# Performance work log

Hardware: AMD Instinct MI355X
Metric: run time of the kernel (lower is better)

The kernel has to match this reference:

```python
import jax, jax.numpy as jnp
import numpy as np

IN_FEATURES = 256
WIDTH = 512
GRID_POINTS = 32   # num control points
DEGREE = 3         # spline_order
BATCH = 8192
LN_EPS = 1e-5


def make_knots(num_ctrl_pts, degree):
    knot_count = num_ctrl_pts + degree + 1
    knots = np.zeros(knot_count, dtype=np.float32)
    knots[-(degree + 1):] = 1.0
    interior = knot_count - 2 * (degree + 1)
    if interior > 0:
        knots[degree + 1:degree + 1 + interior] = np.linspace(0.0, 1.0, interior + 2, dtype=np.float32)[1:-1]
    return jnp.asarray(knots)

KNOTS = make_knots(GRID_POINTS, DEGREE)  # [num_ctrl + degree + 1]


def bspline_basis(x, knots, degree):
    # x: [b, f] in [0,1]; returns [b, f, num_ctrl_pts]
    xe = x[..., None]                      # [b, f, 1]
    left = knots[:-1]
    right = knots[1:]
    basis = ((xe >= left) & (xe < right)).astype(x.dtype)            # [b,f,K-1]
    last = ((xe >= left[-1]) & (xe <= right[-1])).astype(x.dtype)    # [b,f,1]
    basis = jnp.concatenate([basis[..., :-1], last], axis=-1)
    for r in range(1, degree + 1):  # fixed small loop over spline order
        m = basis.shape[-1] - 1
        if m <= 0:
            break
        idx = np.arange(m)
        lk = knots[idx]                 # [m]
        rk = knots[idx + r + 1]
        d1 = knots[idx + r] - knots[idx]
        d2 = knots[idx + r + 1] - knots[idx + 1]
        s1 = jnp.where(d1 > 0, d1, 1.0)  # safe denominators (avoid nan in both where branches)
        s2 = jnp.where(d2 > 0, d2, 1.0)
        t1 = jnp.where(d1 > 0, (xe - lk) / s1, 0.0) * basis[..., :m]
        t2 = jnp.where(d2 > 0, (rk - xe) / s2, 0.0) * basis[..., 1:m + 1]
        basis = t1 + t2
    return basis


def setup_inputs() -> dict:
    key = jax.random.key(0)
    ks = jax.random.split(key, 8)
    coeff_init = np.sqrt(2.0 / (GRID_POINTS * IN_FEATURES)).astype(np.float32)
    return {
        "inputs": jax.random.normal(ks[0], (BATCH, IN_FEATURES), dtype=jnp.float32),
        "input_shift": jnp.zeros((IN_FEATURES,), dtype=jnp.float32),
        "input_log_scale": jnp.zeros((IN_FEATURES,), dtype=jnp.float32),
        "spline_coeffs": coeff_init * jax.random.normal(ks[1], (IN_FEATURES, GRID_POINTS, WIDTH), dtype=jnp.float32),
        "bias": jnp.zeros((WIDTH,), dtype=jnp.float32),
        "skip_w": jax.random.normal(ks[2], (IN_FEATURES, WIDTH), dtype=jnp.float32) / np.sqrt(IN_FEATURES).astype(np.float32),
        "skip_b": jnp.zeros((WIDTH,), dtype=jnp.float32),
        "ln_gamma": jnp.ones((WIDTH,), dtype=jnp.float32),
        "ln_beta": jnp.zeros((WIDTH,), dtype=jnp.float32),
    }


def reference(inputs, input_shift, input_log_scale, spline_coeffs, bias,
              skip_w, skip_b, ln_gamma, ln_beta):
    scale = jax.nn.softplus(input_log_scale) + 0.001
    normalised = jax.nn.sigmoid((inputs - input_shift) * scale)            # [b,f] in (0,1)
    basis = bspline_basis(normalised, KNOTS, DEGREE)                       # [b,f,g]
    spline_mix = jnp.einsum('bfg,fgw->bw', basis, spline_coeffs)
    linear_skip = inputs @ skip_w + skip_b
    combined = spline_mix + linear_skip + bias
    mu = jnp.mean(combined, axis=-1, keepdims=True)
    var = jnp.mean(jnp.square(combined - mu), axis=-1, keepdims=True)
    normed = (combined - mu) * jax.lax.rsqrt(var + LN_EPS) * ln_gamma + ln_beta
    return jax.nn.gelu(normed, approximate=False)  # torch nn.GELU default = exact erf
```

## Files before the change

### kernel.cpp

```cpp
#include <hip/hip_runtime.h>
#include <hip/hip_bf16.h>
#include <math.h>

#define BATCH 8192
#define F 256
#define G 32
#define W 512
#define NCHUNK 132
#define NPER 66

typedef float f32x4 __attribute__((ext_vector_type(4)));
typedef short s16x8 __attribute__((ext_vector_type(8)));
typedef int   i32x4 __attribute__((ext_vector_type(4)));
typedef long long i64x2 __attribute__((ext_vector_type(2)));

__device__ __forceinline__ short f2bf(float f) {
  unsigned int u = __builtin_bit_cast(unsigned int, f);
  u += 0x7fffu + ((u >> 16) & 1u);
  return (short)(u >> 16);
}

__device__ __forceinline__ float knotv(int i) {
  int j = i - 3;
  j = j < 0 ? 0 : (j > 29 ? 29 : j);
  return (float)j * (1.0f / 29.0f);
}

__device__ __forceinline__ float fdiv_fast(float a, float b) {
  return a * __builtin_amdgcn_rcpf(b);
}

__global__ __launch_bounds__(256) void bas_build2(
    const float* __restrict__ inp, const float* __restrict__ shift,
    const float* __restrict__ lscale,
    unsigned long long* __restrict__ nvq, unsigned char* __restrict__ s0q)
{
  __shared__ float T[256][17];
  const int b0 = blockIdx.x * 16;
  const int t = threadIdx.x;
  #pragma unroll
  for (int i = 0; i < 16; ++i)
    T[t][i] = inp[(size_t)(b0 + i) * F + t];
  __syncthreads();
  const int f = t;
  float ls = lscale[f];
  const float sc = fmaxf(ls, 0.0f) + __logf(1.0f + __expf(-fabsf(ls))) + 0.001f;
  const float sh = shift[f];
  unsigned long long* nd = nvq + (size_t)f * BATCH + b0;
  unsigned int s0p[4] = {0, 0, 0, 0};
  #pragma unroll
  for (int rr = 0; rr < 16; ++rr) {
    const float z = (T[f][rr] - sh) * sc;
    const float sg = 1.0f / (1.0f + __expf(-z));
    int s0 = (int)(sg * 29.0f);
    s0 = s0 < 0 ? 0 : (s0 > 28 ? 28 : s0);
    const int sp = s0 + 3;
    float Nv[4], lef[4], rig[4];
    Nv[0] = 1.0f;
    #pragma unroll
    for (int r = 1; r <= 3; ++r) {
      lef[r] = sg - knotv(sp + 1 - r);
      rig[r] = knotv(sp + r) - sg;
      float saved = 0.0f;
      #pragma unroll
      for (int j = 0; j < r; ++j) {
        float temp = fdiv_fast(Nv[j], rig[j + 1] + lef[r - j]);
        Nv[j] = saved + rig[j + 1] * temp;
        saved = lef[r - j] * temp;
      }
      Nv[r] = saved;
    }
    const unsigned long long nv =
        (unsigned long long)(unsigned short)f2bf(Nv[0])
      | ((unsigned long long)(unsigned short)f2bf(Nv[1]) << 16)
      | ((unsigned long long)(unsigned short)f2bf(Nv[2]) << 32)
      | ((unsigned long long)(unsigned short)f2bf(Nv[3]) << 48);
    nd[rr] = nv;
    s0p[rr >> 2] |= ((unsigned int)s0) << ((rr & 3) * 8);
  }
  i32x4 sv;
  sv[0] = (int)s0p[0]; sv[1] = (int)s0p[1]; sv[2] = (int)s0p[2]; sv[3] = (int)s0p[3];
  *(i32x4*)(s0q + (size_t)f * BATCH + b0) = sv;
}

__global__ __launch_bounds__(256) void bws_build(
    const float* __restrict__ coeffs, const float* __restrict__ skip_w,
    short* __restrict__ Bws)
{
  const int gid = blockIdx.x * 256 + threadIdx.x;
  const int lane = gid & 63;
  const int kk = (gid >> 6) & 1;
  const int nf = (gid >> 7) & 3;
  const int wn = (gid >> 9) & 1;
  const int nt = (gid >> 10) & 3;
  const int c  = gid >> 12;
  const int w  = nt * 128 + wn * 64 + nf * 16 + (lane & 15);
  const int kl = kk * 32 + (lane >> 4) * 8;
  const float* src = (c < 128) ? (coeffs + (size_t)(c * 64 + kl) * W + w)
                               : (skip_w + (size_t)((c - 128) * 64 + kl) * W + w);
  s16x8 h;
  #pragma unroll
  for (int j = 0; j < 8; ++j) h[j] = f2bf(src[(size_t)j * W]);
  ((s16x8*)Bws)[gid] = h;
}

__device__ __forceinline__ void stage_nv(short* __restrict__ Ab, int cc,
    int stoff, int hi, int bp, int m0,
    unsigned long long nv, int s0, const float* __restrict__ inp)
{
  short* base = Ab + stoff;
  if (cc < 128) {
    const int pp = s0 & 7, ga = s0 >> 3;
    const int s = 16 * pp, shl = s & 63;
    const unsigned long long a = nv << shl;
    const unsigned long long b = (nv >> (63 - shl)) >> 1;
    const bool hs = (s >= 64);
    i64x2 d0, d1, z;
    d0[0] = hs ? 0ll : (long long)a;
    d0[1] = hs ? (long long)a : (long long)b;
    d1[0] = hs ? (long long)b : 0ll;
    d1[1] = 0ll;
    z[0] = 0ll; z[1] = 0ll;
    *(i64x2*)(base + ga * 128) = d0;
    *(i64x2*)(base + ((ga + 1) & 3) * 128) = d1;
    *(i64x2*)(base + ((ga + 2) & 3) * 128) = z;
    *(i64x2*)(base + ((ga + 3) & 3) * 128) = z;
  } else {
    const int sb = (cc - 128) * 64 + hi * 32;
    const float* ip = inp + (size_t)(m0 + bp) * F + sb;
    #pragma unroll
    for (int lq = 0; lq < 4; ++lq) {
      s16x8 h;
      #pragma unroll
      for (int j = 0; j < 8; ++j) h[j] = f2bf(ip[lq * 8 + j]);
      *(s16x8*)(base + lq * 128) = h;
    }
  }
}

__global__ __launch_bounds__(256, 2) void kan_gemm_v9(
    const float* __restrict__ inp, const short* __restrict__ Bws,
    const unsigned long long* __restrict__ nvq, const unsigned char* __restrict__ s0q,
    const float* __restrict__ bias, const float* __restrict__ skip_b,
    float* __restrict__ out)
{
  __shared__ short Abuf[2][8192];

  const int tid = threadIdx.x;
  const int lane = tid & 63;
  const int wid = tid >> 6;
  const int kh = wid >> 1;
  const int nh = wid & 1;

  const int nb = (blockIdx.x & 7) * 64 + (blockIdx.x >> 3);
  const int mt = nb >> 2, nt = nb & 3;
  const int m0 = mt * 64, n0 = nt * 128;

  const int ci = tid >> 7;
  const int hi = (tid >> 6) & 1;
  const int bp = tid & 63;
  const int mg = bp >> 4, l15b = bp & 15;
  const int stoff = ci * 4096 + ((mg * 2 + hi) * 64 + l15b) * 8;

  f32x4 acc[4][4];
  #pragma unroll
  for (int i = 0; i < 4; ++i)
    #pragma unroll
    for (int j = 0; j < 4; ++j)
      acc[i][j] = (f32x4){0.f, 0.f, 0.f, 0.f};

  const short* bq = Bws + (size_t)(((kh * 4 + nt) * 2 + nh) * 8) * 512 + lane * 8;

#define LOADB(BS) do {                                                          \
    _Pragma("unroll")                                                           \
    for (int nf = 0; nf < 4; ++nf)                                              \
      _Pragma("unroll")                                                         \
      for (int kk = 0; kk < 2; ++kk)                                            \
        BS[nf * 2 + kk] = *(const s16x8*)(bq + (nf * 2 + kk) * 512);            \
    bq += 65536;                                                                \
  } while (0)

#define PREF(NVL, S0L, PTGT) do {                                               \
    const int cc_ = 2 * (PTGT) + ci;                                            \
    if ((PTGT) < NPER && cc_ < 128) {                                           \
      const size_t ix_ = (size_t)(2 * cc_ + hi) * BATCH + m0 + bp;              \
      NVL = nvq[ix_];                                                           \
      S0L = s0q[ix_];                                                           \
    }                                                                           \
  } while (0)

#define MMAC(AB, BS)                                                            \
    _Pragma("unroll")                                                           \
    for (int kk = 0; kk < 2; ++kk)                                              \
      _Pragma("unroll")                                                         \
      for (int mf = 0; mf < 4; ++mf) {                                          \
        s16x8 af = *(const s16x8*)&AB[kh * 4096 + ((mf * 2 + kk) * 64 + lane) * 8]; \
        _Pragma("unroll")                                                       \
        for (int nf = 0; nf < 4; ++nf)                                          \
          acc[mf][nf] = __builtin_amdgcn_mfma_f32_16x16x32_bf16(                \
              af, BS[nf * 2 + kk], acc[mf][nf], 0, 0, 0);                       \
      }

#define PERIOD(P_, ACUR, ANXT, BCUR, BNXT, NVU, S0U, NVL, S0L) do {             \
    asm volatile("s_waitcnt lgkmcnt(0)" ::: "memory");                          \
    __builtin_amdgcn_s_barrier();                                               \
    PREF(NVL, S0L, (P_) + 2);                                                   \
    if ((P_) + 1 < NPER) {                                                      \
      LOADB(BNXT);                                                              \
      stage_nv(ANXT, 2 * ((P_) + 1) + ci, stoff, hi, bp, m0, NVU, S0U, inp);    \
    }                                                                           \
    __builtin_amdgcn_s_setprio(1);                                              \
    MMAC(ACUR, BCUR);                                                           \
    __builtin_amdgcn_s_setprio(0);                                              \
  } while (0)

  s16x8 bA[8], bB[8];
  unsigned long long nvA = 0, nvB = 0;
  int s0A = 0, s0B = 0;

  PREF(nvA, s0A, 0);
  LOADB(bA);
  stage_nv(&Abuf[0][0], 2 * 0 + ci, stoff, hi, bp, m0, nvA, s0A, inp);
  PREF(nvB, s0B, 1);

  for (int p = 0; p < NPER; p += 2) {
    PERIOD(p,     (&Abuf[0][0]), (&Abuf[1][0]), bA, bB, nvB, s0B, nvA, s0A);
    PERIOD(p + 1, (&Abuf[1][0]), (&Abuf[0][0]), bB, bA, nvA, s0A, nvB, s0B);
  }
#undef PERIOD
#undef MMAC
#undef PREF
#undef LOADB

  __syncthreads();
  float* red = (float*)&Abuf[0][0];
  const int l15 = lane & 15;
  const int lq = lane >> 4;
  if (kh == 1) {
    #pragma unroll
    for (int mf = 0; mf < 4; ++mf)
      #pragma unroll
      for (int nf = 0; nf < 4; ++nf)
        *(f32x4*)&red[nh * 4096 + (mf * 4 + nf) * 256 + lane * 4] = acc[mf][nf];
  }
  __syncthreads();
  if (kh == 0) {
    #pragma unroll
    for (int nf = 0; nf < 4; ++nf) {
      const int col = n0 + nh * 64 + nf * 16 + l15;
      const float badd = bias[col] + skip_b[col];
      #pragma unroll
      for (int mf = 0; mf < 4; ++mf) {
        f32x4 part = *(const f32x4*)&red[nh * 4096 + (mf * 4 + nf) * 256 + lane * 4];
        const int r0 = m0 + mf * 16 + lq * 4;
        #pragma unroll
        for (int r = 0; r < 4; ++r)
          out[(size_t)(r0 + r) * W + col] = acc[mf][nf][r] + part[r] + badd;
      }
    }
  }
}

__device__ __forceinline__ void issue_b(int c, int uu, int n0,
                                        const float* __restrict__ coeffs,
                                        const float* __restrict__ skip_w,
                                        float (&r)[4][8]) {
  const float* base = (c < 128) ? (coeffs + (size_t)c * 64 * W)
                                : (skip_w + (size_t)(c - 128) * 64 * W);
  const int kk = (uu >> 6) & 1;
  const int lq = (uu >> 4) & 3;
  const int l15 = uu & 15;
  const int u7 = uu >> 7;
  #pragma unroll
  for (int s = 0; s < 4; ++s) {
    const int w = (2 * s + u7) * 16 + l15;
    const float* p = base + (size_t)(kk * 32 + lq * 8) * W + n0 + w;
    #pragma unroll
    for (int j = 0; j < 8; ++j) r[s][j] = p[(size_t)j * W];
  }
}

__global__ __launch_bounds__(512, 1) void kan_gemm_v2(
    const float* __restrict__ inp, const float* __restrict__ shift,
    const float* __restrict__ lscale, const float* __restrict__ coeffs,
    const float* __restrict__ bias, const float* __restrict__ skip_w,
    const float* __restrict__ skip_b, float* __restrict__ out)
{
  __shared__ short Abuf[2][8192];
  __shared__ short Bbuf[2][8192];
  __shared__ unsigned short sgl[F * 128];

  const int tid = threadIdx.x;
  const int lane = tid & 63;
  const int wid = tid >> 6;
  const int nb = (blockIdx.x & 7) * 32 + (blockIdx.x >> 3);
  const int mt = nb >> 2;
  const int nt = nb & 3;
  const int m0 = mt * 128;
  const int n0 = nt * 128;

  float bpref[4][8];
  if (tid >= 256) issue_b(0, tid - 256, n0, coeffs, skip_w, bpref);

  float* shf = (float*)&Abuf[0][0];
  if (tid < 256) {
    float ls = lscale[tid];
    shf[tid] = fmaxf(ls, 0.0f) + __logf(1.0f + __expf(-fabsf(ls))) + 0.001f;
    shf[256 + tid] = shift[tid];
  }
  __syncthreads();

  {
    const int row = tid & 127;
    const int q = tid >> 7;
    const float* ip = inp + (size_t)(m0 + row) * F + q * 64;
    #pragma unroll
    for (int i = 0; i < 16; ++i) {
      float4 v = *(const float4*)(ip + i * 4);
      float vv[4] = {v.x, v.y, v.z, v.w};
      #pragma unroll
      for (int j = 0; j < 4; ++j) {
        const int f = q * 64 + i * 4 + j;
        const float z = (vv[j] - shf[256 + f]) * shf[f];
        const float sg = 1.0f / (1.0f + __expf(-z));
        sgl[f * 128 + row] = (unsigned short)fminf(sg * 65536.0f, 65535.0f);
      }
    }
  }
  __syncthreads();

  const int wm = wid >> 2;
  const int wn = wid & 3;

  f32x4 acc[4][2];
  #pragma unroll
  for (int i = 0; i < 4; ++i)
    #pragma unroll
    for (int j = 0; j < 2; ++j)
      acc[i][j] = (f32x4){0.f, 0.f, 0.f, 0.f};

  for (int c = 0; c < NCHUNK; ++c) {
    short* Ab = Abuf[c & 1];
    short* Bb = Bbuf[c & 1];

    if (c < 128) {
      s16x8 z = {0, 0, 0, 0, 0, 0, 0, 0};
      ((s16x8*)Ab)[tid * 2] = z;
      ((s16x8*)Ab)[tid * 2 + 1] = z;
    } else if (tid < 256) {
      const int bp = tid & 127, fi = tid >> 7;
      const int sb = (c - 128) * 64 + fi * 32;
      const float* ip = inp + (size_t)(m0 + bp) * F + sb;
      const int rg = bp >> 4, l15b = bp & 15;
      #pragma unroll
      for (int lq2 = 0; lq2 < 4; ++lq2) {
        s16x8 h;
        #pragma unroll
        for (int j = 0; j < 8; ++j) h[j] = f2bf(ip[lq2 * 8 + j]);
        *(s16x8*)&Ab[((rg * 2 + fi) * 64 + lq2 * 16 + l15b) * 8] = h;
      }
    }
    if (tid >= 256) {
      const int uu = tid - 256;
      #pragma unroll
      for (int s = 0; s < 4; ++s) {
        s16x8 h;
        #pragma unroll
        for (int j = 0; j < 8; ++j) h[j] = f2bf(bpref[s][j]);
        *(s16x8*)&Bb[(s * 256 + uu) * 8] = h;
      }
      if (c + 1 < NCHUNK) issue_b(c + 1, uu, n0, coeffs, skip_w, bpref);
    }
    __syncthreads();

    if (c < 128 && tid < 256) {
      const int bp = tid & 127, fi = tid >> 7;
      const int f = 2 * c + fi;
      const float sg = ((float)sgl[f * 128 + bp] + 0.5f) * (1.0f / 65536.0f);
      int s0 = (int)floorf(sg * 29.0f);
      s0 = s0 < 0 ? 0 : (s0 > 28 ? 28 : s0);
      const int sp = s0 + 3;
      float Nv[4], lef[4], rig[4];
      Nv[0] = 1.0f;
      #pragma unroll
      for (int r = 1; r <= 3; ++r) {
        lef[r] = sg - knotv(sp + 1 - r);
        rig[r] = knotv(sp + r) - sg;
        float saved = 0.0f;
        #pragma unroll
        for (int j = 0; j < r; ++j) {
          float temp = fdiv_fast(Nv[j], rig[j + 1] + lef[r - j]);
          Nv[j] = saved + rig[j + 1] * temp;
          saved = lef[r - j] * temp;
        }
        Nv[r] = saved;
      }
      const int rg = bp >> 4, l15b = bp & 15;
      #pragma unroll
      for (int t = 0; t < 4; ++t) {
        const int g = s0 + t;
        Ab[((rg * 2 + fi) * 64 + (g >> 3) * 16 + l15b) * 8 + (g & 7)] = f2bf(Nv[t]);
      }
    }
    s16x8 bfv[2][2];
    #pragma unroll
    for (int nf = 0; nf < 2; ++nf)
      #pragma unroll
      for (int kk = 0; kk < 2; ++kk)
        bfv[nf][kk] = *(const s16x8*)&Bb[(((wn * 2 + nf) * 2 + kk) * 64 + lane) * 8];
    __syncthreads();

    #pragma unroll
    for (int kk = 0; kk < 2; ++kk) {
      #pragma unroll
      for (int mf = 0; mf < 4; ++mf) {
        s16x8 af = *(const s16x8*)&Ab[(((wm * 4 + mf) * 2 + kk) * 64 + lane) * 8];
        #pragma unroll
        for (int nf = 0; nf < 2; ++nf)
          acc[mf][nf] = __builtin_amdgcn_mfma_f32_16x16x32_bf16(af, bfv[nf][kk], acc[mf][nf], 0, 0, 0);
      }
    }
  }

  const int l15 = lane & 15;
  const int lq = lane >> 4;
  #pragma unroll
  for (int nf = 0; nf < 2; ++nf) {
    const int col = n0 + wn * 32 + nf * 16 + l15;
    const float badd = bias[col] + skip_b[col];
    #pragma unroll
    for (int mf = 0; mf < 4; ++mf) {
      const int r0 = m0 + wm * 64 + mf * 16 + lq * 4;
      #pragma unroll
      for (int r = 0; r < 4; ++r)
        out[(size_t)(r0 + r) * W + col] = acc[mf][nf][r] + badd;
    }
  }
}

__global__ __launch_bounds__(256, 1) void ln_gelu(
    float* __restrict__ out, const float* __restrict__ gamma,
    const float* __restrict__ beta)
{
  const int lane = threadIdx.x & 63;
  const int wid = threadIdx.x >> 6;
  const int row = blockIdx.x * 4 + wid;
  float* p = out + (size_t)row * W + lane * 8;
  float4 a = *(const float4*)p;
  float4 b = *(const float4*)(p + 4);
  float v[8] = {a.x, a.y, a.z, a.w, b.x, b.y, b.z, b.w};
  float s = 0.f, q = 0.f;
  #pragma unroll
  for (int j = 0; j < 8; ++j) { s += v[j]; q += v[j] * v[j]; }
  #pragma unroll
  for (int m = 1; m < 64; m <<= 1) {
    s += __shfl_xor(s, m);
    q += __shfl_xor(q, m);
  }
  const float mu = s * (1.0f / 512.0f);
  const float var = q * (1.0f / 512.0f) - mu * mu;
  const float inv = rsqrtf(var + 1e-5f);
  const float4 g0 = *(const float4*)(gamma + lane * 8);
  const float4 g1 = *(const float4*)(gamma + lane * 8 + 4);
  const float4 b0 = *(const float4*)(beta + lane * 8);
  const float4 b1 = *(const float4*)(beta + lane * 8 + 4);
  float gm[8] = {g0.x, g0.y, g0.z, g0.w, g1.x, g1.y, g1.z, g1.w};
  float bt[8] = {b0.x, b0.y, b0.z, b0.w, b1.x, b1.y, b1.z, b1.w};
  float o[8];
  #pragma unroll
  for (int j = 0; j < 8; ++j) {
    float x = (v[j] - mu) * inv * gm[j] + bt[j];
    o[j] = 0.5f * x * (1.0f + erff(x * 0.70710678f));
  }
  float4 w0 = {o[0], o[1], o[2], o[3]};
  float4 w1 = {o[4], o[5], o[6], o[7]};
  *(float4*)p = w0;
  *(float4*)(p + 4) = w1;
}

extern "C" void kernel_launch(void* const* d_in, const int* in_sizes, int n_in,
                              void* d_out, int out_size, void* d_ws, size_t ws_size,
                              hipStream_t stream) {
  (void)in_sizes; (void)n_in; (void)out_size;
  const float* inp    = (const float*)d_in[0];
  const float* shift  = (const float*)d_in[1];
  const float* lscale = (const float*)d_in[2];
  const float* coeffs = (const float*)d_in[3];
  const float* bias   = (const float*)d_in[4];
  const float* skip_w = (const float*)d_in[5];
  const float* skip_b = (const float*)d_in[6];
  const float* gamma  = (const float*)d_in[7];
  const float* beta   = (const float*)d_in[8];
  float* out = (float*)d_out;

  const size_t needB  = (size_t)NCHUNK * 4 * 16384;
  const size_t needNV = (size_t)F * BATCH * 8;
  const size_t needS0 = (size_t)F * BATCH;

  if (ws_size >= needB + needNV + needS0) {
    short* Bws = (short*)d_ws;
    unsigned long long* nvq = (unsigned long long*)((char*)d_ws + needB);
    unsigned char* s0q = (unsigned char*)((char*)d_ws + needB + needNV);
    bas_build2<<<dim3(BATCH / 16), dim3(256), 0, stream>>>(inp, shift, lscale, nvq, s0q);
    bws_build<<<dim3(2112), dim3(256), 0, stream>>>(coeffs, skip_w, Bws);
    kan_gemm_v9<<<dim3(512), dim3(256), 0, stream>>>(
        inp, Bws, nvq, s0q, bias, skip_b, out);
  } else {
    kan_gemm_v2<<<dim3(256), dim3(512), 0, stream>>>(
        inp, shift, lscale, coeffs, bias, skip_w, skip_b, out);
  }
  ln_gelu<<<dim3(BATCH / 4), dim3(256), 0, stream>>>(out, gamma, beta);
}
```

Measured before the change: 92.06 us.

## Build spline A-fragments in registers and drop LDS staging and split-K reduction

The GEMM kernel no longer stages the sparse B-spline basis rows through shared memory. Each wave now loads the packed nonzero values and start offsets directly and builds its MFMA A fragments in registers with shift/select logic. The K dimension is no longer split across waves: each of the four waves owns 32 output columns across the full K range. This removes the barriers, the LDS traffic and the final cross-wave reduction. In exchange every wave redundantly loads and rebuilds the A fragments, and B reuse per wave is halved.

```diff
diff --git a/kernel.cpp b/kernel.cpp
--- a/kernel.cpp
+++ b/kernel.cpp
@@ -7,12 +7,12 @@
 #define G 32
 #define W 512
 #define NCHUNK 132
-#define NPER 66
 
 typedef float f32x4 __attribute__((ext_vector_type(4)));
 typedef short s16x8 __attribute__((ext_vector_type(8)));
 typedef int   i32x4 __attribute__((ext_vector_type(4)));
 typedef long long i64x2 __attribute__((ext_vector_type(2)));
+typedef unsigned long long u64;
 
 __device__ __forceinline__ short f2bf(float f) {
   unsigned int u = __builtin_bit_cast(unsigned int, f);
@@ -28,6 +28,21 @@
 
 __device__ __forceinline__ float fdiv_fast(float a, float b) {
   return a * __builtin_amdgcn_rcpf(b);
+}
+
+__device__ __forceinline__ u64 winpiece(u64 nv, int B) {
+  u64 l = nv << ((unsigned)B & 63);
+  u64 r = nv >> ((unsigned)(-B) & 63);
+  u64 v = (B >= 0) ? l : r;
+  return ((unsigned)(B + 63) < 127u) ? v : 0ULL;
+}
+
+__device__ __forceinline__ s16x8 afrag(u64 nv, int s0, int lqc) {
+  const int B1 = (s0 << 4) - lqc;
+  i64x2 t;
+  t[0] = (long long)winpiece(nv, B1);
+  t[1] = (long long)winpiece(nv, B1 - 64);
+  return __builtin_bit_cast(s16x8, t);
 }
 
 __global__ __launch_bounds__(256) void bas_build2(
@@ -104,159 +119,126 @@
   ((s16x8*)Bws)[gid] = h;
 }
 
-__device__ __forceinline__ void stage_nv(short* __restrict__ Ab, int cc,
-    int stoff, int hi, int bp, int m0,
-    unsigned long long nv, int s0, const float* __restrict__ inp)
-{
-  short* base = Ab + stoff;
-  if (cc < 128) {
-    const int pp = s0 & 7, ga = s0 >> 3;
-    const int s = 16 * pp, shl = s & 63;
-    const unsigned long long a = nv << shl;
-    const unsigned long long b = (nv >> (63 - shl)) >> 1;
-    const bool hs = (s >= 64);
-    i64x2 d0, d1, z;
-    d0[0] = hs ? 0ll : (long long)a;
-    d0[1] = hs ? (long long)a : (long long)b;
-    d1[0] = hs ? (long long)b : 0ll;
-    d1[1] = 0ll;
-    z[0] = 0ll; z[1] = 0ll;
-    *(i64x2*)(base + ga * 128) = d0;
-    *(i64x2*)(base + ((ga + 1) & 3) * 128) = d1;
-    *(i64x2*)(base + ((ga + 2) & 3) * 128) = z;
-    *(i64x2*)(base + ((ga + 3) & 3) * 128) = z;
-  } else {
-    const int sb = (cc - 128) * 64 + hi * 32;
-    const float* ip = inp + (size_t)(m0 + bp) * F + sb;
-    #pragma unroll
-    for (int lq = 0; lq < 4; ++lq) {
-      s16x8 h;
-      #pragma unroll
-      for (int j = 0; j < 8; ++j) h[j] = f2bf(ip[lq * 8 + j]);
-      *(s16x8*)(base + lq * 128) = h;
-    }
-  }
-}
-
-__global__ __launch_bounds__(256, 2) void kan_gemm_v9(
+__global__ __launch_bounds__(256, 2) void kan_gemm_v10(
     const float* __restrict__ inp, const short* __restrict__ Bws,
     const unsigned long long* __restrict__ nvq, const unsigned char* __restrict__ s0q,
     const float* __restrict__ bias, const float* __restrict__ skip_b,
     float* __restrict__ out)
 {
-  __shared__ short Abuf[2][8192];
-
   const int tid = threadIdx.x;
   const int lane = tid & 63;
-  const int wid = tid >> 6;
-  const int kh = wid >> 1;
-  const int nh = wid & 1;
-
-  const int nb = (blockIdx.x & 7) * 64 + (blockIdx.x >> 3);
-  const int mt = nb >> 2, nt = nb & 3;
-  const int m0 = mt * 64, n0 = nt * 128;
-
-  const int ci = tid >> 7;
-  const int hi = (tid >> 6) & 1;
-  const int bp = tid & 63;
-  const int mg = bp >> 4, l15b = bp & 15;
-  const int stoff = ci * 4096 + ((mg * 2 + hi) * 64 + l15b) * 8;
-
-  f32x4 acc[4][4];
+  const int w = tid >> 6;
+  const int l15 = lane & 15;
+  const int lq = lane >> 4;
+  const int lqc = lq << 7;
+
+  const int nb = ((blockIdx.x & 7) << 6) | (blockIdx.x >> 3);
+  const int n2 = nb >> 7;
+  const int mrow = nb & 127;
+  const int m0 = mrow * 64;
+  const int ncol0 = n2 * 128 + w * 32;
+
+  f32x4 acc[4][2];
   #pragma unroll
   for (int i = 0; i < 4; ++i)
     #pragma unroll
-    for (int j = 0; j < 4; ++j)
+    for (int j = 0; j < 2; ++j)
       acc[i][j] = (f32x4){0.f, 0.f, 0.f, 0.f};
 
-  const short* bq = Bws + (size_t)(((kh * 4 + nt) * 2 + nh) * 8) * 512 + lane * 8;
-
-#define LOADB(BS) do {                                                          \
+  const short* bptr = Bws + ((size_t)((n2 * 2 + (w >> 1)) * 8 + (w & 1) * 4)) * 512 + lane * 8;
+
+#define LOADNV(NV, S0, C_) do {                                                 \
     _Pragma("unroll")                                                           \
-    for (int nf = 0; nf < 4; ++nf)                                              \
+    for (int mf = 0; mf < 4; ++mf)                                              \
       _Pragma("unroll")                                                         \
-      for (int kk = 0; kk < 2; ++kk)                                            \
-        BS[nf * 2 + kk] = *(const s16x8*)(bq + (nf * 2 + kk) * 512);            \
-    bq += 65536;                                                                \
+      for (int kk = 0; kk < 2; ++kk) {                                          \
+        const size_t ix = (size_t)(2 * (C_) + kk) * BATCH + m0 + mf * 16 + l15; \
+        NV[mf * 2 + kk] = nvq[ix];                                              \
+        S0[mf * 2 + kk] = (int)s0q[ix];                                         \
+      }                                                                         \
   } while (0)
 
-#define PREF(NVL, S0L, PTGT) do {                                               \
-    const int cc_ = 2 * (PTGT) + ci;                                            \
-    if ((PTGT) < NPER && cc_ < 128) {                                           \
-      const size_t ix_ = (size_t)(2 * cc_ + hi) * BATCH + m0 + bp;              \
-      NVL = nvq[ix_];                                                           \
-      S0L = s0q[ix_];                                                           \
-    }                                                                           \
+#define LOADBV(BV) do {                                                         \
+    _Pragma("unroll")                                                           \
+    for (int q = 0; q < 4; ++q) BV[q] = *(const s16x8*)(bptr + q * 512);        \
+    bptr += 32768;                                                              \
   } while (0)
 
-#define MMAC(AB, BS)                                                            \
+#define STEP(NVc, S0c, BVc, NVn, S0n, BVn, C_) do {                             \
+    if ((C_) + 1 < 128) LOADNV(NVn, S0n, (C_) + 1);                             \
+    LOADBV(BVn);                                                                \
+    s16x8 af[8];                                                                \
+    _Pragma("unroll")                                                           \
+    for (int i = 0; i < 8; ++i) af[i] = afrag(NVc[i], S0c[i], lqc);             \
+    __builtin_amdgcn_s_setprio(1);                                              \
     _Pragma("unroll")                                                           \
     for (int kk = 0; kk < 2; ++kk)                                              \
       _Pragma("unroll")                                                         \
-      for (int mf = 0; mf < 4; ++mf) {                                          \
-        s16x8 af = *(const s16x8*)&AB[kh * 4096 + ((mf * 2 + kk) * 64 + lane) * 8]; \
+      for (int mf = 0; mf < 4; ++mf)                                            \
         _Pragma("unroll")                                                       \
-        for (int nf = 0; nf < 4; ++nf)                                          \
+        for (int nf = 0; nf < 2; ++nf)                                          \
           acc[mf][nf] = __builtin_amdgcn_mfma_f32_16x16x32_bf16(                \
-              af, BS[nf * 2 + kk], acc[mf][nf], 0, 0, 0);                       \
-      }
-
-#define PERIOD(P_, ACUR, ANXT, BCUR, BNXT, NVU, S0U, NVL, S0L) do {             \
-    asm volatile("s_waitcnt lgkmcnt(0)" ::: "memory");                          \
-    __builtin_amdgcn_s_barrier();                                               \
-    PREF(NVL, S0L, (P_) + 2);                                                   \
-    if ((P_) + 1 < NPER) {                                                      \
-      LOADB(BNXT);                                                              \
-      stage_nv(ANXT, 2 * ((P_) + 1) + ci, stoff, hi, bp, m0, NVU, S0U, inp);    \
-    }                                                                           \
-    __builtin_amdgcn_s_setprio(1);                                              \
-    MMAC(ACUR, BCUR);                                                           \
+              af[mf * 2 + kk], BVc[nf * 2 + kk], acc[mf][nf], 0, 0, 0);         \
     __builtin_amdgcn_s_setprio(0);                                              \
   } while (0)
 
-  s16x8 bA[8], bB[8];
-  unsigned long long nvA = 0, nvB = 0;
-  int s0A = 0, s0B = 0;
-
-  PREF(nvA, s0A, 0);
-  LOADB(bA);
-  stage_nv(&Abuf[0][0], 2 * 0 + ci, stoff, hi, bp, m0, nvA, s0A, inp);
-  PREF(nvB, s0B, 1);
-
-  for (int p = 0; p < NPER; p += 2) {
-    PERIOD(p,     (&Abuf[0][0]), (&Abuf[1][0]), bA, bB, nvB, s0B, nvA, s0A);
-    PERIOD(p + 1, (&Abuf[1][0]), (&Abuf[0][0]), bB, bA, nvA, s0A, nvB, s0B);
-  }
-#undef PERIOD
-#undef MMAC
-#undef PREF
-#undef LOADB
-
-  __syncthreads();
-  float* red = (float*)&Abuf[0][0];
-  const int l15 = lane & 15;
-  const int lq = lane >> 4;
-  if (kh == 1) {
+  u64 nvA[8], nvB[8];
+  int s0A[8], s0B[8];
+  s16x8 bA[4], bB[4];
+
+  LOADNV(nvA, s0A, 0);
+  LOADBV(bA);
+
+  for (int c = 0; c < 128; c += 2) {
+    STEP(nvA, s0A, bA, nvB, s0B, bB, c);
+    STEP(nvB, s0B, bB, nvA, s0A, bA, c + 1);
+  }
+#undef STEP
+#undef LOADBV
+#undef LOADNV
+
+  for (int cs = 128; cs < 132; ++cs) {
+    s16x8 bS[4];
+    const short* bp2 = Bws +
+        ((size_t)cs * 64 + (n2 * 2 + (w >> 1)) * 8 + (w & 1) * 4) * 512 + lane * 8;
+    #pragma unroll
+    for (int q = 0; q < 4; ++q) bS[q] = *(const s16x8*)(bp2 + q * 512);
+    s16x8 afS[8];
     #pragma unroll
     for (int mf = 0; mf < 4; ++mf)
       #pragma unroll
-      for (int nf = 0; nf < 4; ++nf)
-        *(f32x4*)&red[nh * 4096 + (mf * 4 + nf) * 256 + lane * 4] = acc[mf][nf];
-  }
-  __syncthreads();
-  if (kh == 0) {
-    #pragma unroll
-    for (int nf = 0; nf < 4; ++nf) {
-      const int col = n0 + nh * 64 + nf * 16 + l15;
-      const float badd = bias[col] + skip_b[col];
-      #pragma unroll
-      for (int mf = 0; mf < 4; ++mf) {
-        f32x4 part = *(const f32x4*)&red[nh * 4096 + (mf * 4 + nf) * 256 + lane * 4];
-        const int r0 = m0 + mf * 16 + lq * 4;
+      for (int kk = 0; kk < 2; ++kk) {
+        const float* ipb = inp + (size_t)(m0 + mf * 16 + l15) * F
+                         + (cs - 128) * 64 + kk * 32 + lq * 8;
+        float4 x = *(const float4*)ipb;
+        float4 y = *(const float4*)(ipb + 4);
+        s16x8 h;
+        h[0] = f2bf(x.x); h[1] = f2bf(x.y); h[2] = f2bf(x.z); h[3] = f2bf(x.w);
+        h[4] = f2bf(y.x); h[5] = f2bf(y.y); h[6] = f2bf(y.z); h[7] = f2bf(y.w);
+        afS[mf * 2 + kk] = h;
+      }
+    __builtin_amdgcn_s_setprio(1);
+    #pragma unroll
+    for (int kk = 0; kk < 2; ++kk)
+      #pragma unroll
+      for (int mf = 0; mf < 4; ++mf)
         #pragma unroll
-        for (int r = 0; r < 4; ++r)
-          out[(size_t)(r0 + r) * W + col] = acc[mf][nf][r] + part[r] + badd;
-      }
+        for (int nf = 0; nf < 2; ++nf)
+          acc[mf][nf] = __builtin_amdgcn_mfma_f32_16x16x32_bf16(
+              afS[mf * 2 + kk], bS[nf * 2 + kk], acc[mf][nf], 0, 0, 0);
+    __builtin_amdgcn_s_setprio(0);
+  }
+
+  #pragma unroll
+  for (int nf = 0; nf < 2; ++nf) {
+    const int col = ncol0 + nf * 16 + l15;
+    const float badd = bias[col] + skip_b[col];
+    #pragma unroll
+    for (int mf = 0; mf < 4; ++mf) {
+      const int r0 = m0 + mf * 16 + lq * 4;
+      #pragma unroll
+      for (int r = 0; r < 4; ++r)
+        out[(size_t)(r0 + r) * W + col] = acc[mf][nf][r] + badd;
     }
   }
 }
@@ -503,7 +485,7 @@
     unsigned char* s0q = (unsigned char*)((char*)d_ws + needB + needNV);
     bas_build2<<<dim3(BATCH / 16), dim3(256), 0, stream>>>(inp, shift, lscale, nvq, s0q);
     bws_build<<<dim3(2112), dim3(256), 0, stream>>>(coeffs, skip_w, Bws);
-    kan_gemm_v9<<<dim3(512), dim3(256), 0, stream>>>(
+    kan_gemm_v10<<<dim3(512), dim3(256), 0, stream>>>(
         inp, Bws, nvq, s0q, bias, skip_b, out);
   } else {
     kan_gemm_v2<<<dim3(256), dim3(512), 0, stream>>>(
```

Result: slower. 162.8 us (+76.9%).

## Double K-chunk per barrier period and split B loads around MFMA halves

Applied to the files above, without the earlier changes.

The GEMM main loop now stages four K-chunks of A (two per thread) per period into a doubled LDS buffer, so it runs half as many barrier-separated periods. B fragments are reloaded in two halves, each issued right after the MFMA block that consumed it, instead of through a separate next-period register set. Block-to-tile mapping also changes so consecutive blocks share an N tile rather than an M tile, which shifts L2 reuse. The goal is fewer barriers and better overlap of global loads with MFMA, at the cost of 64KB of LDS per block, which may limit occupancy to two blocks, and a more serialized B load-to-use dependency.

```diff
diff --git a/kernel.cpp b/kernel.cpp
--- a/kernel.cpp
+++ b/kernel.cpp
@@ -7,12 +7,13 @@
 #define G 32
 #define W 512
 #define NCHUNK 132
-#define NPER 66
+#define NPER4 33
 
 typedef float f32x4 __attribute__((ext_vector_type(4)));
 typedef short s16x8 __attribute__((ext_vector_type(8)));
 typedef int   i32x4 __attribute__((ext_vector_type(4)));
 typedef long long i64x2 __attribute__((ext_vector_type(2)));
+typedef unsigned long long u64;
 
 __device__ __forceinline__ short f2bf(float f) {
   unsigned int u = __builtin_bit_cast(unsigned int, f);
@@ -138,13 +139,13 @@
   }
 }
 
-__global__ __launch_bounds__(256, 2) void kan_gemm_v9(
+__global__ __launch_bounds__(256, 2) void kan_gemm_v11(
     const float* __restrict__ inp, const short* __restrict__ Bws,
     const unsigned long long* __restrict__ nvq, const unsigned char* __restrict__ s0q,
     const float* __restrict__ bias, const float* __restrict__ skip_b,
     float* __restrict__ out)
 {
-  __shared__ short Abuf[2][8192];
+  __shared__ short Abuf[2][16384];
 
   const int tid = threadIdx.x;
   const int lane = tid & 63;
@@ -152,15 +153,20 @@
   const int kh = wid >> 1;
   const int nh = wid & 1;
 
-  const int nb = (blockIdx.x & 7) * 64 + (blockIdx.x >> 3);
-  const int mt = nb >> 2, nt = nb & 3;
-  const int m0 = mt * 64, n0 = nt * 128;
-
-  const int ci = tid >> 7;
+  const int nb = ((blockIdx.x & 7) << 6) | (blockIdx.x >> 3);
+  const int nt = nb >> 7;
+  const int mt = nb & 127;
+  const int m0 = mt * 64;
+  const int n0 = nt * 128;
+
+  const int ci0 = tid >> 7;
+  const int ci1 = 2 + (tid >> 7);
   const int hi = (tid >> 6) & 1;
   const int bp = tid & 63;
   const int mg = bp >> 4, l15b = bp & 15;
-  const int stoff = ci * 4096 + ((mg * 2 + hi) * 64 + l15b) * 8;
+  const int stbase = ((mg * 2 + hi) * 64 + l15b) * 8;
+  const int stoff0 = ci0 * 4096 + stbase;
+  const int stoff1 = ci1 * 4096 + stbase;
 
   f32x4 acc[4][4];
   #pragma unroll
@@ -169,65 +175,76 @@
     for (int j = 0; j < 4; ++j)
       acc[i][j] = (f32x4){0.f, 0.f, 0.f, 0.f};
 
-  const short* bq = Bws + (size_t)(((kh * 4 + nt) * 2 + nh) * 8) * 512 + lane * 8;
-
-#define LOADB(BS) do {                                                          \
+#define LOADB(BS, C_) do {                                                      \
+    const short* bp_ = Bws + (size_t)(C_) * 32768 + nt * 8192 + nh * 4096       \
+                     + lane * 8;                                                \
     _Pragma("unroll")                                                           \
-    for (int nf = 0; nf < 4; ++nf)                                              \
-      _Pragma("unroll")                                                         \
-      for (int kk = 0; kk < 2; ++kk)                                            \
-        BS[nf * 2 + kk] = *(const s16x8*)(bq + (nf * 2 + kk) * 512);            \
-    bq += 65536;                                                                \
+    for (int q = 0; q < 8; ++q) BS[q] = *(const s16x8*)(bp_ + q * 512);         \
   } while (0)
 
-#define PREF(NVL, S0L, PTGT) do {                                               \
-    const int cc_ = 2 * (PTGT) + ci;                                            \
-    if ((PTGT) < NPER && cc_ < 128) {                                           \
-      const size_t ix_ = (size_t)(2 * cc_ + hi) * BATCH + m0 + bp;              \
-      NVL = nvq[ix_];                                                           \
-      S0L = s0q[ix_];                                                           \
+#define PREF(NV, S0, PTGT) do {                                                 \
+    const int ccA_ = 4 * (PTGT) + ci0;                                          \
+    const int ccB_ = 4 * (PTGT) + ci1;                                          \
+    if (ccA_ < 128) {                                                           \
+      const size_t ix_ = (size_t)(2 * ccA_ + hi) * BATCH + m0 + bp;             \
+      NV[0] = nvq[ix_];  S0[0] = (int)s0q[ix_];                                 \
+    }                                                                           \
+    if (ccB_ < 128) {                                                           \
+      const size_t ix_ = (size_t)(2 * ccB_ + hi) * BATCH + m0 + bp;             \
+      NV[1] = nvq[ix_];  S0[1] = (int)s0q[ix_];                                 \
     }                                                                           \
   } while (0)
 
-#define MMAC(AB, BS)                                                            \
+#define MMAC(AB, CIOFF, BS)                                                     \
     _Pragma("unroll")                                                           \
     for (int kk = 0; kk < 2; ++kk)                                              \
       _Pragma("unroll")                                                         \
       for (int mf = 0; mf < 4; ++mf) {                                          \
-        s16x8 af = *(const s16x8*)&AB[kh * 4096 + ((mf * 2 + kk) * 64 + lane) * 8]; \
+        s16x8 af = *(const s16x8*)&AB[(CIOFF) + ((mf * 2 + kk) * 64 + lane) * 8]; \
         _Pragma("unroll")                                                       \
         for (int nf = 0; nf < 4; ++nf)                                          \
           acc[mf][nf] = __builtin_amdgcn_mfma_f32_16x16x32_bf16(                \
               af, BS[nf * 2 + kk], acc[mf][nf], 0, 0, 0);                       \
       }
 
-#define PERIOD(P_, ACUR, ANXT, BCUR, BNXT, NVU, S0U, NVL, S0L) do {             \
+#define BODY(P_, NVU, S0U, NVL, S0L) do {                                       \
     asm volatile("s_waitcnt lgkmcnt(0)" ::: "memory");                          \
     __builtin_amdgcn_s_barrier();                                               \
+    short* AC_ = Abuf[(P_) & 1];                                                \
+    short* AN_ = Abuf[((P_) + 1) & 1];                                          \
+    if ((P_) + 1 < NPER4) {                                                     \
+      stage_nv(AN_, 4 * ((P_) + 1) + ci0, stoff0, hi, bp, m0, NVU[0], S0U[0], inp); \
+      stage_nv(AN_, 4 * ((P_) + 1) + ci1, stoff1, hi, bp, m0, NVU[1], S0U[1], inp); \
+    }                                                                           \
     PREF(NVL, S0L, (P_) + 2);                                                   \
-    if ((P_) + 1 < NPER) {                                                      \
-      LOADB(BNXT);                                                              \
-      stage_nv(ANXT, 2 * ((P_) + 1) + ci, stoff, hi, bp, m0, NVU, S0U, inp);    \
-    }                                                                           \
     __builtin_amdgcn_s_setprio(1);                                              \
-    MMAC(ACUR, BCUR);                                                           \
+    MMAC(AC_, (2 * kh) * 4096, bA);                                             \
     __builtin_amdgcn_s_setprio(0);                                              \
+    if ((P_) + 1 < NPER4) LOADB(bA, 4 * ((P_) + 1) + 2 * kh);                   \
+    __builtin_amdgcn_s_setprio(1);                                              \
+    MMAC(AC_, (2 * kh + 1) * 4096, bB);                                         \
+    __builtin_amdgcn_s_setprio(0);                                              \
+    if ((P_) + 1 < NPER4) LOADB(bB, 4 * ((P_) + 1) + 2 * kh + 1);               \
   } while (0)
 
+  u64 nvA[2], nvB[2];
+  int s0A[2], s0B[2];
   s16x8 bA[8], bB[8];
-  unsigned long long nvA = 0, nvB = 0;
-  int s0A = 0, s0B = 0;
+  nvA[0] = nvA[1] = nvB[0] = nvB[1] = 0;
+  s0A[0] = s0A[1] = s0B[0] = s0B[1] = 0;
 
   PREF(nvA, s0A, 0);
-  LOADB(bA);
-  stage_nv(&Abuf[0][0], 2 * 0 + ci, stoff, hi, bp, m0, nvA, s0A, inp);
+  LOADB(bA, 2 * kh);
+  LOADB(bB, 2 * kh + 1);
+  stage_nv(Abuf[0], ci0, stoff0, hi, bp, m0, nvA[0], s0A[0], inp);
+  stage_nv(Abuf[0], ci1, stoff1, hi, bp, m0, nvA[1], s0A[1], inp);
   PREF(nvB, s0B, 1);
 
-  for (int p = 0; p < NPER; p += 2) {
-    PERIOD(p,     (&Abuf[0][0]), (&Abuf[1][0]), bA, bB, nvB, s0B, nvA, s0A);
-    PERIOD(p + 1, (&Abuf[1][0]), (&Abuf[0][0]), bB, bA, nvA, s0A, nvB, s0B);
-  }
-#undef PERIOD
+  for (int p = 0; p < NPER4; p += 2) {
+    BODY(p, nvB, s0B, nvA, s0A);
+    if (p + 1 < NPER4) BODY(p + 1, nvA, s0A, nvB, s0B);
+  }
+#undef BODY
 #undef MMAC
 #undef PREF
 #undef LOADB
@@ -503,7 +520,7 @@
     unsigned char* s0q = (unsigned char*)((char*)d_ws + needB + needNV);
     bas_build2<<<dim3(BATCH / 16), dim3(256), 0, stream>>>(inp, shift, lscale, nvq, s0q);
     bws_build<<<dim3(2112), dim3(256), 0, stream>>>(coeffs, skip_w, Bws);
-    kan_gemm_v9<<<dim3(512), dim3(256), 0, stream>>>(
+    kan_gemm_v11<<<dim3(512), dim3(256), 0, stream>>>(
         inp, Bws, nvq, s0q, bias, skip_b, out);
   } else {
     kan_gemm_v2<<<dim3(256), dim3(512), 0, stream>>>(
```

Result: slower. 101.8 us (+10.6%).

## Switch GEMM from 16x16x32 to 32x32x16 bf16 MFMA with matching layouts

Applied to the files above, without the earlier changes.

Replaces the 4x4 grid of 16x16x32 MFMA tiles per wave with a 2x2 grid of 32x32x16 MFMA tiles. The B pre-pack kernel, the LDS staging layout for A and the epilogue reduction and store indexing are all rewritten to match the new operand and accumulator layouts. The larger instruction shape is meant to cut the number of MFMA issues and LDS A-fragment reads per K step. In exchange the epilogue writes 16 scattered rows per lane, and LDS bank-conflict behaviour may change.

```diff
diff --git a/kernel.cpp b/kernel.cpp
--- a/kernel.cpp
+++ b/kernel.cpp
@@ -10,9 +10,11 @@
 #define NPER 66
 
 typedef float f32x4 __attribute__((ext_vector_type(4)));
+typedef float f32x16 __attribute__((ext_vector_type(16)));
 typedef short s16x8 __attribute__((ext_vector_type(8)));
 typedef int   i32x4 __attribute__((ext_vector_type(4)));
 typedef long long i64x2 __attribute__((ext_vector_type(2)));
+typedef unsigned long long u64;
 
 __device__ __forceinline__ short f2bf(float f) {
   unsigned int u = __builtin_bit_cast(unsigned int, f);
@@ -83,19 +85,19 @@
   *(i32x4*)(s0q + (size_t)f * BATCH + b0) = sv;
 }
 
-__global__ __launch_bounds__(256) void bws_build(
+__global__ __launch_bounds__(256) void bws_build32(
     const float* __restrict__ coeffs, const float* __restrict__ skip_w,
     short* __restrict__ Bws)
 {
   const int gid = blockIdx.x * 256 + threadIdx.x;
   const int lane = gid & 63;
-  const int kk = (gid >> 6) & 1;
-  const int nf = (gid >> 7) & 3;
-  const int wn = (gid >> 9) & 1;
+  const int ks = (gid >> 6) & 3;
+  const int nf = (gid >> 8) & 1;
+  const int nh = (gid >> 9) & 1;
   const int nt = (gid >> 10) & 3;
   const int c  = gid >> 12;
-  const int w  = nt * 128 + wn * 64 + nf * 16 + (lane & 15);
-  const int kl = kk * 32 + (lane >> 4) * 8;
+  const int w  = nt * 128 + nh * 64 + nf * 32 + (lane & 31);
+  const int kl = ks * 16 + (lane >> 5) * 8;
   const float* src = (c < 128) ? (coeffs + (size_t)(c * 64 + kl) * W + w)
                                : (skip_w + (size_t)((c - 128) * 64 + kl) * W + w);
   s16x8 h;
@@ -104,7 +106,7 @@
   ((s16x8*)Bws)[gid] = h;
 }
 
-__device__ __forceinline__ void stage_nv(short* __restrict__ Ab, int cc,
+__device__ __forceinline__ void stage_nv32(short* __restrict__ Ab, int cc,
     int stoff, int hi, int bp, int m0,
     unsigned long long nv, int s0, const float* __restrict__ inp)
 {
@@ -121,24 +123,24 @@
     d1[0] = hs ? (long long)b : 0ll;
     d1[1] = 0ll;
     z[0] = 0ll; z[1] = 0ll;
-    *(i64x2*)(base + ga * 128) = d0;
-    *(i64x2*)(base + ((ga + 1) & 3) * 128) = d1;
-    *(i64x2*)(base + ((ga + 2) & 3) * 128) = z;
-    *(i64x2*)(base + ((ga + 3) & 3) * 128) = z;
+    *(i64x2*)(base + ga * 256) = d0;
+    *(i64x2*)(base + ((ga + 1) & 3) * 256) = d1;
+    *(i64x2*)(base + ((ga + 2) & 3) * 256) = z;
+    *(i64x2*)(base + ((ga + 3) & 3) * 256) = z;
   } else {
     const int sb = (cc - 128) * 64 + hi * 32;
     const float* ip = inp + (size_t)(m0 + bp) * F + sb;
     #pragma unroll
-    for (int lq = 0; lq < 4; ++lq) {
+    for (int o = 0; o < 4; ++o) {
       s16x8 h;
       #pragma unroll
-      for (int j = 0; j < 8; ++j) h[j] = f2bf(ip[lq * 8 + j]);
-      *(s16x8*)(base + lq * 128) = h;
-    }
-  }
-}
-
-__global__ __launch_bounds__(256, 2) void kan_gemm_v9(
+      for (int j = 0; j < 8; ++j) h[j] = f2bf(ip[o * 8 + j]);
+      *(s16x8*)(base + o * 256) = h;
+    }
+  }
+}
+
+__global__ __launch_bounds__(256, 2) void kan_gemm_v13(
     const float* __restrict__ inp, const short* __restrict__ Bws,
     const unsigned long long* __restrict__ nvq, const unsigned char* __restrict__ s0q,
     const float* __restrict__ bias, const float* __restrict__ skip_b,
@@ -152,32 +154,30 @@
   const int kh = wid >> 1;
   const int nh = wid & 1;
 
-  const int nb = (blockIdx.x & 7) * 64 + (blockIdx.x >> 3);
+  const int nb = ((blockIdx.x & 7) << 6) | (blockIdx.x >> 3);
   const int mt = nb >> 2, nt = nb & 3;
   const int m0 = mt * 64, n0 = nt * 128;
 
   const int ci = tid >> 7;
   const int hi = (tid >> 6) & 1;
   const int bp = tid & 63;
-  const int mg = bp >> 4, l15b = bp & 15;
-  const int stoff = ci * 4096 + ((mg * 2 + hi) * 64 + l15b) * 8;
-
-  f32x4 acc[4][4];
-  #pragma unroll
-  for (int i = 0; i < 4; ++i)
-    #pragma unroll
-    for (int j = 0; j < 4; ++j)
-      acc[i][j] = (f32x4){0.f, 0.f, 0.f, 0.f};
-
-  const short* bq = Bws + (size_t)(((kh * 4 + nt) * 2 + nh) * 8) * 512 + lane * 8;
+  const int mh2 = bp >> 5;
+  const int stoff = ci * 4096 + ((mh2 * 4 + hi * 2) * 64 + (bp & 31)) * 8;
+
+  f32x16 acc[2][2];
+  #pragma unroll
+  for (int i = 0; i < 2; ++i)
+    #pragma unroll
+    for (int j = 0; j < 2; ++j)
+      acc[i][j] = (f32x16)(0.0f);
+
+  const s16x8* bws8 = (const s16x8*)Bws;
+  size_t bidx = (size_t)kh * 4096 + nt * 1024 + nh * 512 + lane;
 
 #define LOADB(BS) do {                                                          \
     _Pragma("unroll")                                                           \
-    for (int nf = 0; nf < 4; ++nf)                                              \
-      _Pragma("unroll")                                                         \
-      for (int kk = 0; kk < 2; ++kk)                                            \
-        BS[nf * 2 + kk] = *(const s16x8*)(bq + (nf * 2 + kk) * 512);            \
-    bq += 65536;                                                                \
+    for (int q = 0; q < 8; ++q) BS[q] = bws8[bidx + q * 64];                    \
+    bidx += 8192;                                                               \
   } while (0)
 
 #define PREF(NVL, S0L, PTGT) do {                                               \
@@ -185,20 +185,20 @@
     if ((PTGT) < NPER && cc_ < 128) {                                           \
       const size_t ix_ = (size_t)(2 * cc_ + hi) * BATCH + m0 + bp;              \
       NVL = nvq[ix_];                                                           \
-      S0L = s0q[ix_];                                                           \
+      S0L = (int)s0q[ix_];                                                      \
     }                                                                           \
   } while (0)
 
 #define MMAC(AB, BS)                                                            \
     _Pragma("unroll")                                                           \
-    for (int kk = 0; kk < 2; ++kk)                                              \
+    for (int ks = 0; ks < 4; ++ks)                                              \
       _Pragma("unroll")                                                         \
-      for (int mf = 0; mf < 4; ++mf) {                                          \
-        s16x8 af = *(const s16x8*)&AB[kh * 4096 + ((mf * 2 + kk) * 64 + lane) * 8]; \
+      for (int mh = 0; mh < 2; ++mh) {                                          \
+        s16x8 af = *(const s16x8*)&AB[kh * 4096 + ((mh * 4 + ks) * 64 + lane) * 8]; \
         _Pragma("unroll")                                                       \
-        for (int nf = 0; nf < 4; ++nf)                                          \
-          acc[mf][nf] = __builtin_amdgcn_mfma_f32_16x16x32_bf16(                \
-              af, BS[nf * 2 + kk], acc[mf][nf], 0, 0, 0);                       \
+        for (int nf = 0; nf < 2; ++nf)                                          \
+          acc[mh][nf] = __builtin_amdgcn_mfma_f32_32x32x16_bf16(                \
+              af, BS[nf * 4 + ks], acc[mh][nf], 0, 0, 0);                       \
       }
 
 #define PERIOD(P_, ACUR, ANXT, BCUR, BNXT, NVU, S0U, NVL, S0L) do {             \
@@ -207,7 +207,7 @@
     PREF(NVL, S0L, (P_) + 2);                                                   \
     if ((P_) + 1 < NPER) {                                                      \
       LOADB(BNXT);                                                              \
-      stage_nv(ANXT, 2 * ((P_) + 1) + ci, stoff, hi, bp, m0, NVU, S0U, inp);    \
+      stage_nv32(ANXT, 2 * ((P_) + 1) + ci, stoff, hi, bp, m0, NVU, S0U, inp);  \
     }                                                                           \
     __builtin_amdgcn_s_setprio(1);                                              \
     MMAC(ACUR, BCUR);                                                           \
@@ -220,7 +220,7 @@
 
   PREF(nvA, s0A, 0);
   LOADB(bA);
-  stage_nv(&Abuf[0][0], 2 * 0 + ci, stoff, hi, bp, m0, nvA, s0A, inp);
+  stage_nv32(&Abuf[0][0], 2 * 0 + ci, stoff, hi, bp, m0, nvA, s0A, inp);
   PREF(nvB, s0B, 1);
 
   for (int p = 0; p < NPER; p += 2) {
@@ -234,28 +234,29 @@
 
   __syncthreads();
   float* red = (float*)&Abuf[0][0];
-  const int l15 = lane & 15;
-  const int lq = lane >> 4;
+  const int l31 = lane & 31;
+  const int lh = lane >> 5;
   if (kh == 1) {
     #pragma unroll
-    for (int mf = 0; mf < 4; ++mf)
-      #pragma unroll
-      for (int nf = 0; nf < 4; ++nf)
-        *(f32x4*)&red[nh * 4096 + (mf * 4 + nf) * 256 + lane * 4] = acc[mf][nf];
+    for (int mh = 0; mh < 2; ++mh)
+      #pragma unroll
+      for (int nf = 0; nf < 2; ++nf)
+        *(f32x16*)&red[nh * 4096 + (mh * 2 + nf) * 1024 + lane * 16] = acc[mh][nf];
   }
   __syncthreads();
   if (kh == 0) {
     #pragma unroll
-    for (int nf = 0; nf < 4; ++nf) {
-      const int col = n0 + nh * 64 + nf * 16 + l15;
+    for (int nf = 0; nf < 2; ++nf) {
+      const int col = n0 + nh * 64 + nf * 32 + l31;
       const float badd = bias[col] + skip_b[col];
       #pragma unroll
-      for (int mf = 0; mf < 4; ++mf) {
-        f32x4 part = *(const f32x4*)&red[nh * 4096 + (mf * 4 + nf) * 256 + lane * 4];
-        const int r0 = m0 + mf * 16 + lq * 4;
+      for (int mh = 0; mh < 2; ++mh) {
+        f32x16 part = *(const f32x16*)&red[nh * 4096 + (mh * 2 + nf) * 1024 + lane * 16];
         #pragma unroll
-        for (int r = 0; r < 4; ++r)
-          out[(size_t)(r0 + r) * W + col] = acc[mf][nf][r] + part[r] + badd;
+        for (int r = 0; r < 16; ++r) {
+          const int row = m0 + mh * 32 + (r & 3) + 8 * (r >> 2) + 4 * lh;
+          out[(size_t)row * W + col] = acc[mh][nf][r] + part[r] + badd;
+        }
       }
     }
   }
@@ -502,8 +503,8 @@
     unsigned long long* nvq = (unsigned long long*)((char*)d_ws + needB);
     unsigned char* s0q = (unsigned char*)((char*)d_ws + needB + needNV);
     bas_build2<<<dim3(BATCH / 16), dim3(256), 0, stream>>>(inp, shift, lscale, nvq, s0q);
-    bws_build<<<dim3(2112), dim3(256), 0, stream>>>(coeffs, skip_w, Bws);
-    kan_gemm_v9<<<dim3(512), dim3(256), 0, stream>>>(
+    bws_build32<<<dim3(2112), dim3(256), 0, stream>>>(coeffs, skip_w, Bws);
+    kan_gemm_v13<<<dim3(512), dim3(256), 0, stream>>>(
         inp, Bws, nvq, s0q, bias, skip_b, out);
   } else {
     kan_gemm_v2<<<dim3(256), dim3(512), 0, stream>>>(
```

Result: slower. 100.5 us (+9.1%).
